# Kernel optimization log

Measured on AMD Instinct MI355X. Metric: run time of the kernel, lower is better.

The kernel has to match this reference:

```python
import jax, jax.numpy as jnp
import numpy as np

B, N, HS = 2, 2048, 1024
H, D = 16, 64
GRID = 16           # crop_size // patch_size
SEG = 20            # d_dim = h_dim = w_dim = 2*(64//3//2)


def setup_inputs() -> dict:
    key = jax.random.key(0)
    ks = jax.random.split(key, 5)
    s = 0.02
    return {
        "hidden_states": jax.random.normal(ks[0], (B, N, HS), jnp.float32),
        "Wq": jax.random.normal(ks[1], (HS, HS), jnp.float32) * s,
        "bq": jnp.zeros((HS,), jnp.float32),
        "Wk": jax.random.normal(ks[2], (HS, HS), jnp.float32) * s,
        "bk": jnp.zeros((HS,), jnp.float32),
        "Wv": jax.random.normal(ks[3], (HS, HS), jnp.float32) * s,
        "bv": jnp.zeros((HS,), jnp.float32),
        "Wp": jax.random.normal(ks[4], (HS, HS), jnp.float32) * s,
        "bp": jnp.zeros((HS,), jnp.float32),
    }


def _rope(x, pos):
    # x: [B, H, N, d], pos: [N] int. Faithful to rotate_queries_or_keys:
    # sin/cos are TILED (concat of two copies), rotation is pairwise interleaved.
    d = x.shape[-1]
    omega = 1.0 / (10000.0 ** (jnp.arange(d // 2, dtype=x.dtype) / (d / 2.0)))
    freq = pos.astype(x.dtype)[:, None] * omega          # [N, d/2]
    sin = jnp.tile(jnp.sin(freq), (1, 2))                # [N, d]
    cos = jnp.tile(jnp.cos(freq), (1, 2))
    xp = x.reshape(x.shape[:-1] + (d // 2, 2))
    rot = jnp.stack([-xp[..., 1], xp[..., 0]], axis=-1).reshape(x.shape)
    return x * cos + rot * sin


def _apply_rope3d(qk, fpos, hpos, wpos):
    parts, s = [], 0
    for pos in (fpos, hpos, wpos):
        parts.append(_rope(qk[..., s:s + SEG], pos))
        s += SEG
    parts.append(qk[..., s:])  # pass-through remainder (4 dims)
    return jnp.concatenate(parts, axis=-1)


def reference(hidden_states, Wq, bq, Wk, bk, Wv, bv, Wp, bp):
    b, n, _ = hidden_states.shape

    def heads(x):  # [B,N,HS] -> [B,H,N,D]
        return x.reshape(b, n, H, D).transpose(0, 2, 1, 3)

    q = heads(hidden_states @ Wq.T + bq)
    k = heads(hidden_states @ Wk.T + bk)
    v = heads(hidden_states @ Wv.T + bv)

    ids = jnp.arange(n)
    tpf = GRID * GRID
    fpos = ids // tpf
    rem = ids - fpos * tpf
    hpos = rem // GRID
    wpos = rem - hpos * GRID

    q = _apply_rope3d(q, fpos, hpos, wpos)
    k = _apply_rope3d(k, fpos, hpos, wpos)

    scores = jnp.einsum('bhqd,bhkd->bhqk', q, k) * (D ** -0.5)
    probs = jax.nn.softmax(scores.astype(jnp.float32), axis=-1).astype(q.dtype)
    ctx = jnp.einsum('bhqk,bhkd->bqhd', probs, v).reshape(b, n, HS)
    return ctx @ Wp.T + bp
```

## Files before the change

kernel.cpp:

```cpp
#include <hip/hip_runtime.h>
#include <hip/hip_bf16.h>
#include <math.h>

#define BB    2
#define NN    2048
#define HSZ   1024
#define NH    16
#define HD    64
#define SEGW  20

#define LOG2E  1.4426950408889634f
#define QSCALE (0.125f * LOG2E)
#define DTHR   8.0f

typedef unsigned short u16;
typedef unsigned int   u32;
using bf16x8 = __attribute__((ext_vector_type(8))) short;
using f32x4  = __attribute__((ext_vector_type(4))) float;

__device__ __forceinline__ u16 f2b(float f) {
    union { float f; u32 u; } x; x.f = f;
    u32 r = x.u + 0x7FFF + ((x.u >> 16) & 1);
    return (u16)(r >> 16);
}
__device__ __forceinline__ u16 f2bc(float f) {
    __hip_bfloat16 h = __float2bfloat16(f);
    return *reinterpret_cast<u16*>(&h);
}

__device__ __forceinline__ void gload16(void* lds, const void* g) {
    __builtin_amdgcn_global_load_lds(
        (const __attribute__((address_space(1))) void*)g,
        (__attribute__((address_space(3))) void*)lds, 16, 0, 0);
}

__global__ __launch_bounds__(256)
void cast_k(const float* __restrict__ hs, const float* __restrict__ Wq,
            const float* __restrict__ Wk, const float* __restrict__ Wv,
            const float* __restrict__ Wp, u16* __restrict__ hsb,
            u16* __restrict__ wqb, u16* __restrict__ wkb,
            u16* __restrict__ wvb, u16* __restrict__ wpb) {
    size_t idx = ((size_t)blockIdx.x * 256 + threadIdx.x) * 4;
    const float* s; u16* d; size_t o;
    const size_t HSN = 4194304, WN = 1048576;
    if      (idx < HSN)          { s = hs; d = hsb; o = idx; }
    else if (idx < HSN + WN)     { s = Wq; d = wqb; o = idx - HSN; }
    else if (idx < HSN + 2*WN)   { s = Wk; d = wkb; o = idx - HSN - WN; }
    else if (idx < HSN + 3*WN)   { s = Wv; d = wvb; o = idx - HSN - 2*WN; }
    else                         { s = Wp; d = wpb; o = idx - HSN - 3*WN; }
    float4 v = *(const float4*)(s + o);
    u32 lo = f2b(v.x) | ((u32)f2b(v.y) << 16);
    u32 hi = f2b(v.z) | ((u32)f2b(v.w) << 16);
    *(uint2*)(d + o) = uint2{lo, hi};
}

__global__ void rope_table_k(float* __restrict__ tab) {
    int n = blockIdx.x, d = threadIdx.x;
    float c = 1.f, s = 0.f;
    if (d < 3 * SEGW) {
        int seg = d / SEGW;
        int jj  = (d % SEGW) % (SEGW / 2);
        int rem = n & 255;
        int pos = (seg == 0) ? (n >> 8) : ((seg == 1) ? (rem >> 4) : (rem & 15));
        float omega = powf(10000.f, -(float)jj / 10.f);
        float fr = (float)pos * omega;
        s = sinf(fr); c = cosf(fr);
    }
    tab[(n * 64 + d) * 2 + 0] = c;
    tab[(n * 64 + d) * 2 + 1] = s;
}

__device__ __forceinline__
void gemm_body(const u16* __restrict__ X, const u16* __restrict__ Wb,
               const float* __restrict__ bias, void* __restrict__ out,
               const float* __restrict__ tab, int mode) {
    __shared__ u16 As[2][128 * 32];
    __shared__ u16 Bs[2][128 * 32];

    const int t  = threadIdx.x;
    const int w  = t >> 6;
    const int l  = t & 63;
    const int o0 = blockIdx.x * 128;
    const int m0 = blockIdx.y * 128;
    const int wr = (w >> 1) * 64;
    const int wc = (w & 1) * 64;

    const int ch  = (w << 6) + l;
    const int rA0 = ch >> 2,         cA0 = (((ch & 3) ^ (rA0 & 3))) * 8;
    const int rA1 = (ch + 256) >> 2, cA1 = (((ch & 3) ^ (rA1 & 3))) * 8;
    const int kbyte = (((l >> 4) ^ (l & 3)) << 4);

    f32x4 acc[4][4] = {};

    gload16(As[0] + ((w << 6)) * 8,       X  + (size_t)(m0 + rA0) * HSZ + cA0);
    gload16(As[0] + (256 + (w << 6)) * 8, X  + (size_t)(m0 + rA1) * HSZ + cA1);
    gload16(Bs[0] + ((w << 6)) * 8,       Wb + (size_t)(o0 + rA0) * HSZ + cA0);
    gload16(Bs[0] + (256 + (w << 6)) * 8, Wb + (size_t)(o0 + rA1) * HSZ + cA1);
    __syncthreads();

    int cur = 0;
    for (int k0 = 0; k0 < HSZ; k0 += 32, cur ^= 1) {
        if (k0 + 32 < HSZ) {
            int kn = k0 + 32;
            gload16(As[cur ^ 1] + ((w << 6)) * 8,       X  + (size_t)(m0 + rA0) * HSZ + kn + cA0);
            gload16(As[cur ^ 1] + (256 + (w << 6)) * 8, X  + (size_t)(m0 + rA1) * HSZ + kn + cA1);
            gload16(Bs[cur ^ 1] + ((w << 6)) * 8,       Wb + (size_t)(o0 + rA0) * HSZ + kn + cA0);
            gload16(Bs[cur ^ 1] + (256 + (w << 6)) * 8, Wb + (size_t)(o0 + rA1) * HSZ + kn + cA1);
        }
        bf16x8 af[4], bfr[4];
#pragma unroll
        for (int i = 0; i < 4; ++i) {
            int row = wr + i * 16 + (l & 15);
            af[i] = *(const bf16x8*)((const char*)As[cur] + row * 64 + kbyte);
        }
#pragma unroll
        for (int j = 0; j < 4; ++j) {
            int row = wc + j * 16 + (l & 15);
            bfr[j] = *(const bf16x8*)((const char*)Bs[cur] + row * 64 + kbyte);
        }
        __builtin_amdgcn_s_setprio(1);
#pragma unroll
        for (int i = 0; i < 4; ++i)
#pragma unroll
            for (int j = 0; j < 4; ++j)
                acc[i][j] = __builtin_amdgcn_mfma_f32_16x16x32_bf16(af[i], bfr[j], acc[i][j], 0, 0, 0);
        __builtin_amdgcn_s_setprio(0);
        __syncthreads();
    }

#pragma unroll
    for (int j = 0; j < 4; ++j) {
        int oc = o0 + wc + j * 16 + (l & 15);
        int h  = oc >> 6;
        int d  = oc & 63;
        float bv = bias[oc];
        if (mode == 2) {
#pragma unroll
            for (int rt = 0; rt < 4; ++rt) {
                int base = m0 + wr + rt * 16 + (l >> 4) * 4;
                int b_ = base >> 11, n0 = base & (NN - 1);
                u16 e[4];
#pragma unroll
                for (int r = 0; r < 4; ++r) e[r] = f2b(acc[rt][j][r] + bv);
                u32 lo = e[0] | ((u32)e[1] << 16);
                u32 hi = e[2] | ((u32)e[3] << 16);
                u16* vp = (u16*)out + (((size_t)b_ * NH + h) * HD + d) * NN + n0;
                *(uint2*)vp = uint2{lo, hi};
            }
        } else if (mode == 3) {
#pragma unroll
            for (int rt = 0; rt < 4; ++rt)
#pragma unroll
                for (int r = 0; r < 4; ++r) {
                    int m = m0 + wr + rt * 16 + (l >> 4) * 4 + r;
                    ((float*)out)[(size_t)m * HSZ + oc] = acc[rt][j][r] + bv;
                }
        } else {
            float scl = (mode == 0) ? QSCALE : 1.f;
#pragma unroll
            for (int rt = 0; rt < 4; ++rt)
#pragma unroll
                for (int r = 0; r < 4; ++r) {
                    int m = m0 + wr + rt * 16 + (l >> 4) * 4 + r;
                    int n = m & (NN - 1), b_ = m >> 11;
                    float v = acc[rt][j][r] + bv;
                    float2 cs = ((const float2*)tab)[n * 64 + d];
                    float part = __shfl_xor(v, 1);
                    float vr = (l & 1) ? fmaf(part, cs.y, v * cs.x)
                                       : fmaf(-part, cs.y, v * cs.x);
                    u16* qp = (u16*)out + (((size_t)b_ * NH + h) * NN + n) * HD + d;
                    *qp = f2b(vr * scl);
                }
        }
    }
}

__global__ __launch_bounds__(256)
void qkv_k(const u16* __restrict__ X,
           const u16* __restrict__ Wq, const u16* __restrict__ Wk, const u16* __restrict__ Wv,
           const float* __restrict__ bq, const float* __restrict__ bk, const float* __restrict__ bv,
           u16* __restrict__ qo, u16* __restrict__ ko, u16* __restrict__ vo,
           const float* __restrict__ tab) {
    int z = blockIdx.z;
    const u16* W   = (z == 0) ? Wq : (z == 1) ? Wk : Wv;
    const float* b = (z == 0) ? bq : (z == 1) ? bk : bv;
    u16* o         = (z == 0) ? qo : (z == 1) ? ko : vo;
    gemm_body(X, W, b, o, tab, z);
}

__global__ __launch_bounds__(256)
void projo_k(const u16* __restrict__ X, const u16* __restrict__ W,
             const float* __restrict__ b, float* __restrict__ out) {
    gemm_body(X, W, b, out, nullptr, 3);
}

__global__ __launch_bounds__(256)
void attn_mfma_k(const u16* __restrict__ Qb, const u16* __restrict__ Kb,
                 const u16* __restrict__ Vtb, u16* __restrict__ ctxb) {
    __shared__ u16 QPs[128 * 64];
    __shared__ u16 Ks[2][64 * 64];
    __shared__ u16 Vs[2][64 * 64];

    const int t = threadIdx.x, w = t >> 6, l = t & 63;
    int f  = blockIdx.y * 16 + blockIdx.x;
    int bh = (f & 7) * 4 + ((f >> 3) & 3);
    int qt = f >> 5;
    const int b_ = bh >> 4, h = bh & 15;

    const u16* Qg  = Qb + ((size_t)bh * NN + qt * 128) * HD;
    const u16* Kg0 = Kb + (size_t)bh * NN * HD;
    const u16* Vg0 = Vtb + (size_t)bh * HD * NN;

    const int ch0 = (w << 6) + l;
    const int r0 = ch0 >> 3,         s0 = (ch0 & 7) ^ (r0 & 7);
    const int r1 = (ch0 + 256) >> 3, s1 = (ch0 & 7) ^ (r1 & 7);

#pragma unroll
    for (int s = 0; s < 4; ++s) {
        int c = s * 256 + ch0;
        int row = c >> 3, sc = (c & 7) ^ (row & 7);
        gload16(QPs + (s * 256 + (w << 6)) * 8, Qg + row * HD + sc * 8);
    }
    gload16(Ks[0] + ((w << 6)) * 8,       Kg0 + (size_t)r0 * HD + s0 * 8);
    gload16(Ks[0] + (256 + (w << 6)) * 8, Kg0 + (size_t)r1 * HD + s1 * 8);
    gload16(Vs[0] + ((w << 6)) * 8,       Vg0 + (size_t)r0 * NN + s0 * 8);
    gload16(Vs[0] + (256 + (w << 6)) * 8, Vg0 + (size_t)r1 * NN + s1 * 8);
    __syncthreads();

    bf16x8 qf[2][2];
#pragma unroll
    for (int qs = 0; qs < 2; ++qs)
#pragma unroll
        for (int kk = 0; kk < 2; ++kk) {
            int row = w * 32 + qs * 16 + (l & 15);
            int cb = (kk * 64 + (l >> 4) * 16) ^ ((row & 7) << 4);
            qf[qs][kk] = *(const bf16x8*)((const char*)QPs + row * 128 + cb);
        }
    __syncthreads();

    bf16x8 ones;
#pragma unroll
    for (int i = 0; i < 8; ++i) ones[i] = (short)0x3F80;

    float m_i[2][4], l_i[2][4] = {};
#pragma unroll
    for (int qs = 0; qs < 2; ++qs)
#pragma unroll
        for (int r = 0; r < 4; ++r) m_i[qs][r] = -INFINITY;
    f32x4 o_acc[2][4] = {};

    int cur = 0;
    for (int kt = 0; kt < NN / 64; ++kt, cur ^= 1) {
        if (kt + 1 < NN / 64) {
            const u16* Kg = Kg0 + (size_t)((kt + 1) * 64) * HD;
            const u16* Vg = Vg0 + (kt + 1) * 64;
            gload16(Ks[cur ^ 1] + ((w << 6)) * 8,       Kg + (size_t)r0 * HD + s0 * 8);
            gload16(Ks[cur ^ 1] + (256 + (w << 6)) * 8, Kg + (size_t)r1 * HD + s1 * 8);
            gload16(Vs[cur ^ 1] + ((w << 6)) * 8,       Vg + (size_t)r0 * NN + s0 * 8);
            gload16(Vs[cur ^ 1] + (256 + (w << 6)) * 8, Vg + (size_t)r1 * NN + s1 * 8);
        }

        f32x4 sacc[2][4] = {};
        __builtin_amdgcn_s_setprio(1);
#pragma unroll
        for (int ct = 0; ct < 4; ++ct) {
            int row = ct * 16 + (l & 15);
#pragma unroll
            for (int kk = 0; kk < 2; ++kk) {
                int cb = (kk * 64 + (l >> 4) * 16) ^ ((row & 7) << 4);
                bf16x8 kf = *(const bf16x8*)((const char*)Ks[cur] + row * 128 + cb);
                sacc[0][ct] = __builtin_amdgcn_mfma_f32_16x16x32_bf16(qf[0][kk], kf, sacc[0][ct], 0, 0, 0);
                sacc[1][ct] = __builtin_amdgcn_mfma_f32_16x16x32_bf16(qf[1][kk], kf, sacc[1][ct], 0, 0, 0);
            }
        }
        __builtin_amdgcn_s_setprio(0);

        float pm[2][4];
        bool grow = false;
#pragma unroll
        for (int qs = 0; qs < 2; ++qs)
#pragma unroll
            for (int r = 0; r < 4; ++r) {
                pm[qs][r] = fmaxf(fmaxf(sacc[qs][0][r], sacc[qs][1][r]),
                                  fmaxf(sacc[qs][2][r], sacc[qs][3][r]));
                grow = grow | (pm[qs][r] > m_i[qs][r] + DTHR);
            }
        if (__any(grow)) {
#pragma unroll
            for (int qs = 0; qs < 2; ++qs)
#pragma unroll
                for (int r = 0; r < 4; ++r) {
                    float mx = pm[qs][r];
                    mx = fmaxf(mx, __shfl_xor(mx, 1));
                    mx = fmaxf(mx, __shfl_xor(mx, 2));
                    mx = fmaxf(mx, __shfl_xor(mx, 4));
                    mx = fmaxf(mx, __shfl_xor(mx, 8));
                    float mn = fmaxf(m_i[qs][r], mx);
                    float alpha = __builtin_amdgcn_exp2f(m_i[qs][r] - mn);
                    m_i[qs][r] = mn;
                    l_i[qs][r] *= alpha;
#pragma unroll
                    for (int dt = 0; dt < 4; ++dt) o_acc[qs][dt][r] *= alpha;
                }
        }

#pragma unroll
        for (int qs = 0; qs < 2; ++qs)
#pragma unroll
            for (int ct = 0; ct < 4; ++ct)
#pragma unroll
                for (int r = 0; r < 4; ++r) {
                    float p = __builtin_amdgcn_exp2f(sacc[qs][ct][r] - m_i[qs][r]);
                    int row = w * 32 + qs * 16 + (l >> 4) * 4 + r;
                    int cb = ((ct * 16 + (l & 15)) * 2) ^ ((row & 7) << 4);
                    *(u16*)((char*)QPs + row * 128 + cb) = f2bc(p);
                }

        f32x4 lacc[2] = {};
        __builtin_amdgcn_s_setprio(1);
#pragma unroll
        for (int kk = 0; kk < 2; ++kk) {
            bf16x8 pf[2];
#pragma unroll
            for (int qs = 0; qs < 2; ++qs) {
                int prow = w * 32 + qs * 16 + (l & 15);
                int pcb = (kk * 64 + (l >> 4) * 16) ^ ((prow & 7) << 4);
                pf[qs] = *(const bf16x8*)((const char*)QPs + prow * 128 + pcb);
            }
            lacc[0] = __builtin_amdgcn_mfma_f32_16x16x32_bf16(pf[0], ones, lacc[0], 0, 0, 0);
            lacc[1] = __builtin_amdgcn_mfma_f32_16x16x32_bf16(pf[1], ones, lacc[1], 0, 0, 0);
#pragma unroll
            for (int dt = 0; dt < 4; ++dt) {
                int vrow = dt * 16 + (l & 15);
                int vcb = (kk * 64 + (l >> 4) * 16) ^ ((vrow & 7) << 4);
                bf16x8 vf = *(const bf16x8*)((const char*)Vs[cur] + vrow * 128 + vcb);
                o_acc[0][dt] = __builtin_amdgcn_mfma_f32_16x16x32_bf16(pf[0], vf, o_acc[0][dt], 0, 0, 0);
                o_acc[1][dt] = __builtin_amdgcn_mfma_f32_16x16x32_bf16(pf[1], vf, o_acc[1][dt], 0, 0, 0);
            }
        }
        __builtin_amdgcn_s_setprio(0);
#pragma unroll
        for (int qs = 0; qs < 2; ++qs)
#pragma unroll
            for (int r = 0; r < 4; ++r) l_i[qs][r] += lacc[qs][r];

        __syncthreads();
    }

#pragma unroll
    for (int qs = 0; qs < 2; ++qs)
#pragma unroll
        for (int r = 0; r < 4; ++r) {
            float inv = 1.f / l_i[qs][r];
            int n = qt * 128 + w * 32 + qs * 16 + (l >> 4) * 4 + r;
#pragma unroll
            for (int dt = 0; dt < 4; ++dt) {
                int d = dt * 16 + (l & 15);
                ctxb[((size_t)b_ * NN + n) * HSZ + h * HD + d] = f2bc(o_acc[qs][dt][r] * inv);
            }
        }
}

extern "C" void kernel_launch(void* const* d_in, const int* in_sizes, int n_in,
                              void* d_out, int out_size, void* d_ws, size_t ws_size,
                              hipStream_t stream) {
    (void)in_sizes; (void)n_in; (void)out_size; (void)ws_size;
    const float* hs = (const float*)d_in[0];
    const float* Wq = (const float*)d_in[1];
    const float* bq = (const float*)d_in[2];
    const float* Wk = (const float*)d_in[3];
    const float* bk = (const float*)d_in[4];
    const float* Wv = (const float*)d_in[5];
    const float* bv = (const float*)d_in[6];
    const float* Wp = (const float*)d_in[7];
    const float* bp = (const float*)d_in[8];

    char* ws = (char*)d_ws;
    u16*   hsb  = (u16*)(ws);
    u16*   Wqb  = (u16*)(ws + 8388608);
    u16*   Wkb  = (u16*)(ws + 10485760);
    u16*   Wvb  = (u16*)(ws + 12582912);
    u16*   Wpb  = (u16*)(ws + 14680064);
    u16*   qb   = (u16*)(ws + 16777216);
    u16*   kb   = (u16*)(ws + 25165824);
    u16*   vtb  = (u16*)(ws + 33554432);
    u16*   ctxb = (u16*)(ws + 41943040);
    float* tab  = (float*)(ws + 50331648);

    cast_k<<<8192, 256, 0, stream>>>(hs, Wq, Wk, Wv, Wp, hsb, Wqb, Wkb, Wvb, Wpb);
    rope_table_k<<<NN, 64, 0, stream>>>(tab);

    qkv_k<<<dim3(HSZ / 128, (BB * NN) / 128, 3), 256, 0, stream>>>(
        hsb, Wqb, Wkb, Wvb, bq, bk, bv, qb, kb, vtb, tab);

    attn_mfma_k<<<dim3(NN / 128, BB * NH), 256, 0, stream>>>(qb, kb, vtb, ctxb);

    projo_k<<<dim3(HSZ / 128, (BB * NN) / 128), 256, 0, stream>>>(ctxb, Wpb, bp, (float*)d_out);
}
```

Before: 150.9 us.

## Split attention over KV halves with a combine kernel, and swizzle GEMM block order

The attention kernel is split along the key sequence into two halves (blockIdx.z). Each half writes unnormalized fp32 partial outputs plus its row max and sum, and a new combine kernel merges them into the bf16 context. Key tiles shrink to 32, LDS use drops, and launch bounds request 4 blocks per CU, all to raise occupancy and parallelism over the previous 512-block grid. The Wp cast moves after attention so its buffer can reuse workspace, and GEMM block indices are remapped for cache locality. The cost is extra fp32 partial traffic and two extra kernel launches.

```diff
diff --git a/kernel.cpp b/kernel.cpp
--- a/kernel.cpp
+++ b/kernel.cpp
@@ -37,21 +37,28 @@
 __global__ __launch_bounds__(256)
 void cast_k(const float* __restrict__ hs, const float* __restrict__ Wq,
             const float* __restrict__ Wk, const float* __restrict__ Wv,
-            const float* __restrict__ Wp, u16* __restrict__ hsb,
-            u16* __restrict__ wqb, u16* __restrict__ wkb,
-            u16* __restrict__ wvb, u16* __restrict__ wpb) {
+            u16* __restrict__ hsb, u16* __restrict__ wqb,
+            u16* __restrict__ wkb, u16* __restrict__ wvb) {
     size_t idx = ((size_t)blockIdx.x * 256 + threadIdx.x) * 4;
     const float* s; u16* d; size_t o;
     const size_t HSN = 4194304, WN = 1048576;
     if      (idx < HSN)          { s = hs; d = hsb; o = idx; }
     else if (idx < HSN + WN)     { s = Wq; d = wqb; o = idx - HSN; }
     else if (idx < HSN + 2*WN)   { s = Wk; d = wkb; o = idx - HSN - WN; }
-    else if (idx < HSN + 3*WN)   { s = Wv; d = wvb; o = idx - HSN - 2*WN; }
-    else                         { s = Wp; d = wpb; o = idx - HSN - 3*WN; }
+    else                         { s = Wv; d = wvb; o = idx - HSN - 2*WN; }
     float4 v = *(const float4*)(s + o);
     u32 lo = f2b(v.x) | ((u32)f2b(v.y) << 16);
     u32 hi = f2b(v.z) | ((u32)f2b(v.w) << 16);
     *(uint2*)(d + o) = uint2{lo, hi};
+}
+
+__global__ __launch_bounds__(256)
+void castwp_k(const float* __restrict__ Wp, u16* __restrict__ wpb) {
+    size_t idx = ((size_t)blockIdx.x * 256 + threadIdx.x) * 4;
+    float4 v = *(const float4*)(Wp + idx);
+    u32 lo = f2b(v.x) | ((u32)f2b(v.y) << 16);
+    u32 hi = f2b(v.z) | ((u32)f2b(v.w) << 16);
+    *(uint2*)(wpb + idx) = uint2{lo, hi};
 }
 
 __global__ void rope_table_k(float* __restrict__ tab) {
@@ -80,8 +87,9 @@
     const int t  = threadIdx.x;
     const int w  = t >> 6;
     const int l  = t & 63;
-    const int o0 = blockIdx.x * 128;
-    const int m0 = blockIdx.y * 128;
+    const int flat = blockIdx.x + (blockIdx.y << 3);
+    const int o0 = (flat >> 5) * 128;
+    const int m0 = (flat & 31) * 128;
     const int wr = (w >> 1) * 64;
     const int wc = (w & 1) * 64;
 
@@ -194,37 +202,39 @@
     gemm_body(X, W, b, out, nullptr, 3);
 }
 
-__global__ __launch_bounds__(256)
+__global__ __launch_bounds__(256, 4)
 void attn_mfma_k(const u16* __restrict__ Qb, const u16* __restrict__ Kb,
-                 const u16* __restrict__ Vtb, u16* __restrict__ ctxb) {
+                 const u16* __restrict__ Vtb, float* __restrict__ po0,
+                 float* __restrict__ po1, float* __restrict__ pm,
+                 float* __restrict__ pl) {
     __shared__ u16 QPs[128 * 64];
-    __shared__ u16 Ks[2][64 * 64];
-    __shared__ u16 Vs[2][64 * 64];
+    __shared__ u16 Ks[2][32 * 64];
+    __shared__ u16 Vs[2][64 * 32];
 
     const int t = threadIdx.x, w = t >> 6, l = t & 63;
     int f  = blockIdx.y * 16 + blockIdx.x;
     int bh = (f & 7) * 4 + ((f >> 3) & 3);
     int qt = f >> 5;
-    const int b_ = bh >> 4, h = bh & 15;
+    const int sp = blockIdx.z;
+    float* po = sp ? po1 : po0;
+    const int kt0 = sp * 32;
 
     const u16* Qg  = Qb + ((size_t)bh * NN + qt * 128) * HD;
     const u16* Kg0 = Kb + (size_t)bh * NN * HD;
     const u16* Vg0 = Vtb + (size_t)bh * HD * NN;
 
-    const int ch0 = (w << 6) + l;
-    const int r0 = ch0 >> 3,         s0 = (ch0 & 7) ^ (r0 & 7);
-    const int r1 = (ch0 + 256) >> 3, s1 = (ch0 & 7) ^ (r1 & 7);
+    const int ch   = (w << 6) + l;
+    const int krow = ch >> 3, ksc = (ch & 7) ^ (krow & 7);
+    const int vrow = ch >> 2, vsc = (ch & 3) ^ (vrow & 3);
 
 #pragma unroll
     for (int s = 0; s < 4; ++s) {
-        int c = s * 256 + ch0;
+        int c = s * 256 + ch;
         int row = c >> 3, sc = (c & 7) ^ (row & 7);
         gload16(QPs + (s * 256 + (w << 6)) * 8, Qg + row * HD + sc * 8);
     }
-    gload16(Ks[0] + ((w << 6)) * 8,       Kg0 + (size_t)r0 * HD + s0 * 8);
-    gload16(Ks[0] + (256 + (w << 6)) * 8, Kg0 + (size_t)r1 * HD + s1 * 8);
-    gload16(Vs[0] + ((w << 6)) * 8,       Vg0 + (size_t)r0 * NN + s0 * 8);
-    gload16(Vs[0] + (256 + (w << 6)) * 8, Vg0 + (size_t)r1 * NN + s1 * 8);
+    gload16(Ks[0] + (w << 6) * 8, Kg0 + (size_t)(kt0 * 32 + krow) * HD + ksc * 8);
+    gload16(Vs[0] + (w << 6) * 8, Vg0 + (size_t)vrow * NN + kt0 * 32 + vsc * 8);
     __syncthreads();
 
     bf16x8 qf[2][2];
@@ -236,7 +246,6 @@
             int cb = (kk * 64 + (l >> 4) * 16) ^ ((row & 7) << 4);
             qf[qs][kk] = *(const bf16x8*)((const char*)QPs + row * 128 + cb);
         }
-    __syncthreads();
 
     bf16x8 ones;
 #pragma unroll
@@ -250,20 +259,18 @@
     f32x4 o_acc[2][4] = {};
 
     int cur = 0;
-    for (int kt = 0; kt < NN / 64; ++kt, cur ^= 1) {
-        if (kt + 1 < NN / 64) {
-            const u16* Kg = Kg0 + (size_t)((kt + 1) * 64) * HD;
-            const u16* Vg = Vg0 + (kt + 1) * 64;
-            gload16(Ks[cur ^ 1] + ((w << 6)) * 8,       Kg + (size_t)r0 * HD + s0 * 8);
-            gload16(Ks[cur ^ 1] + (256 + (w << 6)) * 8, Kg + (size_t)r1 * HD + s1 * 8);
-            gload16(Vs[cur ^ 1] + ((w << 6)) * 8,       Vg + (size_t)r0 * NN + s0 * 8);
-            gload16(Vs[cur ^ 1] + (256 + (w << 6)) * 8, Vg + (size_t)r1 * NN + s1 * 8);
-        }
-
-        f32x4 sacc[2][4] = {};
+    for (int kt = kt0; kt < kt0 + 32; ++kt, cur ^= 1) {
+        if (kt + 1 < kt0 + 32) {
+            gload16(Ks[cur ^ 1] + (w << 6) * 8,
+                    Kg0 + (size_t)((kt + 1) * 32 + krow) * HD + ksc * 8);
+            gload16(Vs[cur ^ 1] + (w << 6) * 8,
+                    Vg0 + (size_t)vrow * NN + (kt + 1) * 32 + vsc * 8);
+        }
+
+        f32x4 sacc[2][2] = {};
         __builtin_amdgcn_s_setprio(1);
 #pragma unroll
-        for (int ct = 0; ct < 4; ++ct) {
+        for (int ct = 0; ct < 2; ++ct) {
             int row = ct * 16 + (l & 15);
 #pragma unroll
             for (int kk = 0; kk < 2; ++kk) {
@@ -275,22 +282,21 @@
         }
         __builtin_amdgcn_s_setprio(0);
 
-        float pm[2][4];
+        float pmx[2][4];
         bool grow = false;
 #pragma unroll
         for (int qs = 0; qs < 2; ++qs)
 #pragma unroll
             for (int r = 0; r < 4; ++r) {
-                pm[qs][r] = fmaxf(fmaxf(sacc[qs][0][r], sacc[qs][1][r]),
-                                  fmaxf(sacc[qs][2][r], sacc[qs][3][r]));
-                grow = grow | (pm[qs][r] > m_i[qs][r] + DTHR);
+                pmx[qs][r] = fmaxf(sacc[qs][0][r], sacc[qs][1][r]);
+                grow = grow | (pmx[qs][r] > m_i[qs][r] + DTHR);
             }
         if (__any(grow)) {
 #pragma unroll
             for (int qs = 0; qs < 2; ++qs)
 #pragma unroll
                 for (int r = 0; r < 4; ++r) {
-                    float mx = pm[qs][r];
+                    float mx = pmx[qs][r];
                     mx = fmaxf(mx, __shfl_xor(mx, 1));
                     mx = fmaxf(mx, __shfl_xor(mx, 2));
                     mx = fmaxf(mx, __shfl_xor(mx, 4));
@@ -307,7 +313,7 @@
 #pragma unroll
         for (int qs = 0; qs < 2; ++qs)
 #pragma unroll
-            for (int ct = 0; ct < 4; ++ct)
+            for (int ct = 0; ct < 2; ++ct)
 #pragma unroll
                 for (int r = 0; r < 4; ++r) {
                     float p = __builtin_amdgcn_exp2f(sacc[qs][ct][r] - m_i[qs][r]);
@@ -317,48 +323,82 @@
                 }
 
         f32x4 lacc[2] = {};
+        bf16x8 pf[2];
+#pragma unroll
+        for (int qs = 0; qs < 2; ++qs) {
+            int prow = w * 32 + qs * 16 + (l & 15);
+            int pcb = ((l >> 4) * 16) ^ ((prow & 7) << 4);
+            pf[qs] = *(const bf16x8*)((const char*)QPs + prow * 128 + pcb);
+        }
         __builtin_amdgcn_s_setprio(1);
-#pragma unroll
-        for (int kk = 0; kk < 2; ++kk) {
-            bf16x8 pf[2];
-#pragma unroll
-            for (int qs = 0; qs < 2; ++qs) {
-                int prow = w * 32 + qs * 16 + (l & 15);
-                int pcb = (kk * 64 + (l >> 4) * 16) ^ ((prow & 7) << 4);
-                pf[qs] = *(const bf16x8*)((const char*)QPs + prow * 128 + pcb);
+        lacc[0] = __builtin_amdgcn_mfma_f32_16x16x32_bf16(pf[0], ones, lacc[0], 0, 0, 0);
+        lacc[1] = __builtin_amdgcn_mfma_f32_16x16x32_bf16(pf[1], ones, lacc[1], 0, 0, 0);
+#pragma unroll
+        for (int dt = 0; dt < 4; ++dt) {
+            int vr = dt * 16 + (l & 15);
+            int vcb = ((l >> 4) * 16) ^ ((vr & 3) << 4);
+            bf16x8 vf = *(const bf16x8*)((const char*)Vs[cur] + vr * 64 + vcb);
+            o_acc[0][dt] = __builtin_amdgcn_mfma_f32_16x16x32_bf16(pf[0], vf, o_acc[0][dt], 0, 0, 0);
+            o_acc[1][dt] = __builtin_amdgcn_mfma_f32_16x16x32_bf16(pf[1], vf, o_acc[1][dt], 0, 0, 0);
+        }
+        __builtin_amdgcn_s_setprio(0);
+#pragma unroll
+        for (int qs = 0; qs < 2; ++qs)
+#pragma unroll
+            for (int r = 0; r < 4; ++r) l_i[qs][r] += lacc[qs][r];
+
+        __syncthreads();
+    }
+
+#pragma unroll
+    for (int qs = 0; qs < 2; ++qs)
+#pragma unroll
+        for (int r = 0; r < 4; ++r) {
+            int n = qt * 128 + w * 32 + qs * 16 + (l >> 4) * 4 + r;
+#pragma unroll
+            for (int dt = 0; dt < 4; ++dt)
+                po[((size_t)bh * NN + n) * HD + dt * 16 + (l & 15)] = o_acc[qs][dt][r];
+        }
+    if ((l & 15) == 0) {
+#pragma unroll
+        for (int qs = 0; qs < 2; ++qs)
+#pragma unroll
+            for (int r = 0; r < 4; ++r) {
+                int n = qt * 128 + w * 32 + qs * 16 + (l >> 4) * 4 + r;
+                pm[sp * 65536 + bh * NN + n] = m_i[qs][r];
+                pl[sp * 65536 + bh * NN + n] = l_i[qs][r];
             }
-            lacc[0] = __builtin_amdgcn_mfma_f32_16x16x32_bf16(pf[0], ones, lacc[0], 0, 0, 0);
-            lacc[1] = __builtin_amdgcn_mfma_f32_16x16x32_bf16(pf[1], ones, lacc[1], 0, 0, 0);
-#pragma unroll
-            for (int dt = 0; dt < 4; ++dt) {
-                int vrow = dt * 16 + (l & 15);
-                int vcb = (kk * 64 + (l >> 4) * 16) ^ ((vrow & 7) << 4);
-                bf16x8 vf = *(const bf16x8*)((const char*)Vs[cur] + vrow * 128 + vcb);
-                o_acc[0][dt] = __builtin_amdgcn_mfma_f32_16x16x32_bf16(pf[0], vf, o_acc[0][dt], 0, 0, 0);
-                o_acc[1][dt] = __builtin_amdgcn_mfma_f32_16x16x32_bf16(pf[1], vf, o_acc[1][dt], 0, 0, 0);
-            }
-        }
-        __builtin_amdgcn_s_setprio(0);
-#pragma unroll
-        for (int qs = 0; qs < 2; ++qs)
-#pragma unroll
-            for (int r = 0; r < 4; ++r) l_i[qs][r] += lacc[qs][r];
-
-        __syncthreads();
-    }
-
-#pragma unroll
-    for (int qs = 0; qs < 2; ++qs)
-#pragma unroll
-        for (int r = 0; r < 4; ++r) {
-            float inv = 1.f / l_i[qs][r];
-            int n = qt * 128 + w * 32 + qs * 16 + (l >> 4) * 4 + r;
-#pragma unroll
-            for (int dt = 0; dt < 4; ++dt) {
-                int d = dt * 16 + (l & 15);
-                ctxb[((size_t)b_ * NN + n) * HSZ + h * HD + d] = f2bc(o_acc[qs][dt][r] * inv);
-            }
-        }
+    }
+}
+
+__global__ __launch_bounds__(256)
+void combine_k(const float* __restrict__ po0, const float* __restrict__ po1,
+               const float* __restrict__ pm, const float* __restrict__ pl,
+               u16* __restrict__ ctxb) {
+    int idx = blockIdx.x * 256 + threadIdx.x;
+    int row = idx >> 2;
+    int dp  = (idx & 3) * 16;
+    int bh = row >> 11, n = row & 2047;
+    int b_ = bh >> 4, h = bh & 15;
+    float m0 = pm[row], m1 = pm[65536 + row];
+    float l0 = pl[row], l1 = pl[65536 + row];
+    float m = fmaxf(m0, m1);
+    float w0 = __builtin_amdgcn_exp2f(m0 - m);
+    float w1 = __builtin_amdgcn_exp2f(m1 - m);
+    float inv = 1.f / (w0 * l0 + w1 * l1);
+    const float* a = po0 + (size_t)row * 64 + dp;
+    const float* b = po1 + (size_t)row * 64 + dp;
+    u16* o = ctxb + ((size_t)b_ * NN + n) * HSZ + h * 64 + dp;
+#pragma unroll
+    for (int j = 0; j < 4; ++j) {
+        float4 x = ((const float4*)a)[j];
+        float4 y = ((const float4*)b)[j];
+        u16 e0 = f2b((x.x * w0 + y.x * w1) * inv);
+        u16 e1 = f2b((x.y * w0 + y.y * w1) * inv);
+        u16 e2 = f2b((x.z * w0 + y.z * w1) * inv);
+        u16 e3 = f2b((x.w * w0 + y.w * w1) * inv);
+        *(uint2*)(o + j * 4) = uint2{e0 | ((u32)e1 << 16), e2 | ((u32)e3 << 16)};
+    }
 }
 
 extern "C" void kernel_launch(void* const* d_in, const int* in_sizes, int n_in,
@@ -380,20 +420,28 @@
     u16*   Wqb  = (u16*)(ws + 8388608);
     u16*   Wkb  = (u16*)(ws + 10485760);
     u16*   Wvb  = (u16*)(ws + 12582912);
-    u16*   Wpb  = (u16*)(ws + 14680064);
     u16*   qb   = (u16*)(ws + 16777216);
     u16*   kb   = (u16*)(ws + 25165824);
     u16*   vtb  = (u16*)(ws + 33554432);
     u16*   ctxb = (u16*)(ws + 41943040);
     float* tab  = (float*)(ws + 50331648);
-
-    cast_k<<<8192, 256, 0, stream>>>(hs, Wq, Wk, Wv, Wp, hsb, Wqb, Wkb, Wvb, Wpb);
+    float* pm   = (float*)(ws + 50331648);
+    float* pl   = (float*)(ws + 50331648 + 524288);
+    float* po0  = (float*)(ws + 51380224);
+    float* po1  = (float*)(ws);
+    u16*   Wpb  = (u16*)(ws);
+
+    cast_k<<<7168, 256, 0, stream>>>(hs, Wq, Wk, Wv, hsb, Wqb, Wkb, Wvb);
     rope_table_k<<<NN, 64, 0, stream>>>(tab);
 
     qkv_k<<<dim3(HSZ / 128, (BB * NN) / 128, 3), 256, 0, stream>>>(
         hsb, Wqb, Wkb, Wvb, bq, bk, bv, qb, kb, vtb, tab);
 
-    attn_mfma_k<<<dim3(NN / 128, BB * NH), 256, 0, stream>>>(qb, kb, vtb, ctxb);
+    attn_mfma_k<<<dim3(NN / 128, BB * NH, 2), 256, 0, stream>>>(
+        qb, kb, vtb, po0, po1, pm, pl);
+
+    combine_k<<<1024, 256, 0, stream>>>(po0, po1, pm, pl, ctxb);
+    castwp_k<<<1024, 256, 0, stream>>>(Wp, Wpb);
 
     projo_k<<<dim3(HSZ / 128, (BB * NN) / 128), 256, 0, stream>>>(ctxb, Wpb, bp, (float*)d_out);
 }
```

New measurement: 162.1 us. 1.07x slower.

## Rewrite attention with 32x32x16 MFMA, transposed scores and register-resident P

Applied to the files above, without the earlier changes.

The attention kernel now computes transposed scores S^T = K·Q^T using 32x32x16 bf16 MFMA, so each lane owns one query row. The softmax row max and sum then reduce in registers with a single cross-half shuffle. The probabilities are packed into bf16 pairs and rearranged with v_permlane32_swap to feed the PV MFMA directly. This removes the LDS round-trip for P, the ones-vector MFMA used for row sums, and the 16-lane shuffle reductions. The GEMM tile mapping is also remapped so that consecutive blocks share weight columns, which should improve L2 reuse.

```diff
diff --git a/kernel.cpp b/kernel.cpp
--- a/kernel.cpp
+++ b/kernel.cpp
@@ -17,6 +17,7 @@
 typedef unsigned int   u32;
 using bf16x8 = __attribute__((ext_vector_type(8))) short;
 using f32x4  = __attribute__((ext_vector_type(4))) float;
+using f32x16 = __attribute__((ext_vector_type(16))) float;
 
 __device__ __forceinline__ u16 f2b(float f) {
     union { float f; u32 u; } x; x.f = f;
@@ -32,6 +33,10 @@
     __builtin_amdgcn_global_load_lds(
         (const __attribute__((address_space(1))) void*)g,
         (__attribute__((address_space(3))) void*)lds, 16, 0, 0);
+}
+
+__device__ __forceinline__ void pswap(u32& a, u32& b) {
+    asm volatile("v_permlane32_swap_b32 %0, %1" : "+v"(a), "+v"(b));
 }
 
 __global__ __launch_bounds__(256)
@@ -80,8 +85,9 @@
     const int t  = threadIdx.x;
     const int w  = t >> 6;
     const int l  = t & 63;
-    const int o0 = blockIdx.x * 128;
-    const int m0 = blockIdx.y * 128;
+    const int flat = blockIdx.x + (blockIdx.y << 3);
+    const int o0 = (flat >> 5) * 128;
+    const int m0 = (flat & 31) * 128;
     const int wr = (w >> 1) * 64;
     const int wc = (w & 1) * 64;
 
@@ -197,168 +203,147 @@
 __global__ __launch_bounds__(256)
 void attn_mfma_k(const u16* __restrict__ Qb, const u16* __restrict__ Kb,
                  const u16* __restrict__ Vtb, u16* __restrict__ ctxb) {
-    __shared__ u16 QPs[128 * 64];
-    __shared__ u16 Ks[2][64 * 64];
-    __shared__ u16 Vs[2][64 * 64];
+    __shared__ u16 KVs[2][2][64 * 64];
 
     const int t = threadIdx.x, w = t >> 6, l = t & 63;
+    const int h = l >> 5;
     int f  = blockIdx.y * 16 + blockIdx.x;
     int bh = (f & 7) * 4 + ((f >> 3) & 3);
     int qt = f >> 5;
-    const int b_ = bh >> 4, h = bh & 15;
-
-    const u16* Qg  = Qb + ((size_t)bh * NN + qt * 128) * HD;
-    const u16* Kg0 = Kb + (size_t)bh * NN * HD;
-    const u16* Vg0 = Vtb + (size_t)bh * HD * NN;
-
-    const int ch0 = (w << 6) + l;
-    const int r0 = ch0 >> 3,         s0 = (ch0 & 7) ^ (r0 & 7);
-    const int r1 = (ch0 + 256) >> 3, s1 = (ch0 & 7) ^ (r1 & 7);
+    const int b_ = bh >> 4, hd = bh & 15;
+
+    const u16* Qg = Qb + ((size_t)bh * NN + qt * 128) * HD;
+    const u16* Kg = Kb + (size_t)bh * NN * HD;
+    const u16* Vg = Vtb + (size_t)bh * HD * NN;
+
+    const int xr   = (l & 7) << 4;
+    const int h16  = h * 16;
+    const int rowo = (l & 31) * 128;
+    int kb4[4];
+#pragma unroll
+    for (int ks = 0; ks < 4; ++ks) kb4[ks] = ((ks * 32) | h16) ^ xr;
+
+    const int ch  = w * 64 + l;
+    const int r0  = ch >> 3,          sl0 = (ch & 7) ^ (r0 & 7);
+    const int r1  = (ch + 256) >> 3,  sl1 = (ch & 7) ^ (r1 & 7);
 
 #pragma unroll
     for (int s = 0; s < 4; ++s) {
-        int c = s * 256 + ch0;
-        int row = c >> 3, sc = (c & 7) ^ (row & 7);
-        gload16(QPs + (s * 256 + (w << 6)) * 8, Qg + row * HD + sc * 8);
-    }
-    gload16(Ks[0] + ((w << 6)) * 8,       Kg0 + (size_t)r0 * HD + s0 * 8);
-    gload16(Ks[0] + (256 + (w << 6)) * 8, Kg0 + (size_t)r1 * HD + s1 * 8);
-    gload16(Vs[0] + ((w << 6)) * 8,       Vg0 + (size_t)r0 * NN + s0 * 8);
-    gload16(Vs[0] + (256 + (w << 6)) * 8, Vg0 + (size_t)r1 * NN + s1 * 8);
+        int c = s * 256 + ch;
+        int row = c >> 3, sl = (c & 7) ^ (row & 7);
+        gload16(&KVs[0][0][0] + (s * 256 + w * 64) * 8, Qg + row * HD + sl * 8);
+    }
     __syncthreads();
-
-    bf16x8 qf[2][2];
-#pragma unroll
-    for (int qs = 0; qs < 2; ++qs)
-#pragma unroll
-        for (int kk = 0; kk < 2; ++kk) {
-            int row = w * 32 + qs * 16 + (l & 15);
-            int cb = (kk * 64 + (l >> 4) * 16) ^ ((row & 7) << 4);
-            qf[qs][kk] = *(const bf16x8*)((const char*)QPs + row * 128 + cb);
-        }
+    bf16x8 qf[4];
+    {
+        const char* Ql = (const char*)&KVs[0][0][0];
+        int qrow = (w * 32 + (l & 31)) * 128;
+#pragma unroll
+        for (int ks = 0; ks < 4; ++ks)
+            qf[ks] = *(const bf16x8*)(Ql + qrow + kb4[ks]);
+    }
     __syncthreads();
 
-    bf16x8 ones;
-#pragma unroll
-    for (int i = 0; i < 8; ++i) ones[i] = (short)0x3F80;
-
-    float m_i[2][4], l_i[2][4] = {};
-#pragma unroll
-    for (int qs = 0; qs < 2; ++qs)
-#pragma unroll
-        for (int r = 0; r < 4; ++r) m_i[qs][r] = -INFINITY;
-    f32x4 o_acc[2][4] = {};
+    gload16(&KVs[0][0][0] + (w * 64) * 8,        Kg + (size_t)r0 * HD + sl0 * 8);
+    gload16(&KVs[0][0][0] + (256 + w * 64) * 8,  Kg + (size_t)r1 * HD + sl1 * 8);
+    gload16(&KVs[0][1][0] + (w * 64) * 8,        Vg + (size_t)r0 * NN + sl0 * 8);
+    gload16(&KVs[0][1][0] + (256 + w * 64) * 8,  Vg + (size_t)r1 * NN + sl1 * 8);
+    __syncthreads();
+
+    float m_i = -INFINITY, l_i = 0.f;
+    f32x16 oa0 = {}, oa1 = {};
 
     int cur = 0;
     for (int kt = 0; kt < NN / 64; ++kt, cur ^= 1) {
         if (kt + 1 < NN / 64) {
-            const u16* Kg = Kg0 + (size_t)((kt + 1) * 64) * HD;
-            const u16* Vg = Vg0 + (kt + 1) * 64;
-            gload16(Ks[cur ^ 1] + ((w << 6)) * 8,       Kg + (size_t)r0 * HD + s0 * 8);
-            gload16(Ks[cur ^ 1] + (256 + (w << 6)) * 8, Kg + (size_t)r1 * HD + s1 * 8);
-            gload16(Vs[cur ^ 1] + ((w << 6)) * 8,       Vg + (size_t)r0 * NN + s0 * 8);
-            gload16(Vs[cur ^ 1] + (256 + (w << 6)) * 8, Vg + (size_t)r1 * NN + s1 * 8);
-        }
-
-        f32x4 sacc[2][4] = {};
+            int nx = (kt + 1) * 64;
+            gload16(&KVs[cur ^ 1][0][0] + (w * 64) * 8,       Kg + (size_t)(nx + r0) * HD + sl0 * 8);
+            gload16(&KVs[cur ^ 1][0][0] + (256 + w * 64) * 8, Kg + (size_t)(nx + r1) * HD + sl1 * 8);
+            gload16(&KVs[cur ^ 1][1][0] + (w * 64) * 8,       Vg + (size_t)r0 * NN + nx + sl0 * 8);
+            gload16(&KVs[cur ^ 1][1][0] + (256 + w * 64) * 8, Vg + (size_t)r1 * NN + nx + sl1 * 8);
+        }
+
+        const char* Kl = (const char*)&KVs[cur][0][0];
+        f32x16 sa0 = {}, sa1 = {};
         __builtin_amdgcn_s_setprio(1);
 #pragma unroll
-        for (int ct = 0; ct < 4; ++ct) {
-            int row = ct * 16 + (l & 15);
-#pragma unroll
-            for (int kk = 0; kk < 2; ++kk) {
-                int cb = (kk * 64 + (l >> 4) * 16) ^ ((row & 7) << 4);
-                bf16x8 kf = *(const bf16x8*)((const char*)Ks[cur] + row * 128 + cb);
-                sacc[0][ct] = __builtin_amdgcn_mfma_f32_16x16x32_bf16(qf[0][kk], kf, sacc[0][ct], 0, 0, 0);
-                sacc[1][ct] = __builtin_amdgcn_mfma_f32_16x16x32_bf16(qf[1][kk], kf, sacc[1][ct], 0, 0, 0);
-            }
+        for (int ks = 0; ks < 4; ++ks) {
+            bf16x8 k0 = *(const bf16x8*)(Kl + rowo + kb4[ks]);
+            bf16x8 k1 = *(const bf16x8*)(Kl + 4096 + rowo + kb4[ks]);
+            sa0 = __builtin_amdgcn_mfma_f32_32x32x16_bf16(k0, qf[ks], sa0, 0, 0, 0);
+            sa1 = __builtin_amdgcn_mfma_f32_32x32x16_bf16(k1, qf[ks], sa1, 0, 0, 0);
         }
         __builtin_amdgcn_s_setprio(0);
 
-        float pm[2][4];
-        bool grow = false;
-#pragma unroll
-        for (int qs = 0; qs < 2; ++qs)
-#pragma unroll
-            for (int r = 0; r < 4; ++r) {
-                pm[qs][r] = fmaxf(fmaxf(sacc[qs][0][r], sacc[qs][1][r]),
-                                  fmaxf(sacc[qs][2][r], sacc[qs][3][r]));
-                grow = grow | (pm[qs][r] > m_i[qs][r] + DTHR);
-            }
-        if (__any(grow)) {
-#pragma unroll
-            for (int qs = 0; qs < 2; ++qs)
-#pragma unroll
-                for (int r = 0; r < 4; ++r) {
-                    float mx = pm[qs][r];
-                    mx = fmaxf(mx, __shfl_xor(mx, 1));
-                    mx = fmaxf(mx, __shfl_xor(mx, 2));
-                    mx = fmaxf(mx, __shfl_xor(mx, 4));
-                    mx = fmaxf(mx, __shfl_xor(mx, 8));
-                    float mn = fmaxf(m_i[qs][r], mx);
-                    float alpha = __builtin_amdgcn_exp2f(m_i[qs][r] - mn);
-                    m_i[qs][r] = mn;
-                    l_i[qs][r] *= alpha;
-#pragma unroll
-                    for (int dt = 0; dt < 4; ++dt) o_acc[qs][dt][r] *= alpha;
-                }
-        }
-
-#pragma unroll
-        for (int qs = 0; qs < 2; ++qs)
-#pragma unroll
-            for (int ct = 0; ct < 4; ++ct)
-#pragma unroll
-                for (int r = 0; r < 4; ++r) {
-                    float p = __builtin_amdgcn_exp2f(sacc[qs][ct][r] - m_i[qs][r]);
-                    int row = w * 32 + qs * 16 + (l >> 4) * 4 + r;
-                    int cb = ((ct * 16 + (l & 15)) * 2) ^ ((row & 7) << 4);
-                    *(u16*)((char*)QPs + row * 128 + cb) = f2bc(p);
-                }
-
-        f32x4 lacc[2] = {};
+        float mx8[8];
+#pragma unroll
+        for (int j = 0; j < 8; ++j)
+            mx8[j] = fmaxf(fmaxf(sa0[j], sa0[j + 8]), fmaxf(sa1[j], sa1[j + 8]));
+        float pm = fmaxf(fmaxf(fmaxf(mx8[0], mx8[1]), fmaxf(mx8[2], mx8[3])),
+                         fmaxf(fmaxf(mx8[4], mx8[5]), fmaxf(mx8[6], mx8[7])));
+        if (__any(pm > m_i + DTHR)) {
+            float mx = fmaxf(pm, __shfl_xor(pm, 32));
+            float mn = fmaxf(m_i, mx);
+            float alpha = __builtin_amdgcn_exp2f(m_i - mn);
+            m_i = mn;
+            l_i *= alpha;
+#pragma unroll
+            for (int r = 0; r < 16; ++r) { oa0[r] *= alpha; oa1[r] *= alpha; }
+        }
+
+        u32 o_[16];
+        float ls0 = 0.f, ls1 = 0.f, ls2 = 0.f, ls3 = 0.f;
+#pragma unroll
+        for (int j = 0; j < 8; ++j) {
+            float pa = __builtin_amdgcn_exp2f(sa0[2 * j]     - m_i);
+            float pb = __builtin_amdgcn_exp2f(sa0[2 * j + 1] - m_i);
+            float pc = __builtin_amdgcn_exp2f(sa1[2 * j]     - m_i);
+            float pd = __builtin_amdgcn_exp2f(sa1[2 * j + 1] - m_i);
+            ls0 += pa; ls1 += pb; ls2 += pc; ls3 += pd;
+            o_[j]     = (u32)f2bc(pa) | ((u32)f2bc(pb) << 16);
+            o_[8 + j] = (u32)f2bc(pc) | ((u32)f2bc(pd) << 16);
+        }
+        l_i += (ls0 + ls1) + (ls2 + ls3);
+
+        pswap(o_[0], o_[2]);   pswap(o_[1], o_[3]);
+        pswap(o_[4], o_[6]);   pswap(o_[5], o_[7]);
+        pswap(o_[8], o_[10]);  pswap(o_[9], o_[11]);
+        pswap(o_[12], o_[14]); pswap(o_[13], o_[15]);
+
+        const char* Vl = (const char*)&KVs[cur][1][0];
         __builtin_amdgcn_s_setprio(1);
 #pragma unroll
-        for (int kk = 0; kk < 2; ++kk) {
-            bf16x8 pf[2];
-#pragma unroll
-            for (int qs = 0; qs < 2; ++qs) {
-                int prow = w * 32 + qs * 16 + (l & 15);
-                int pcb = (kk * 64 + (l >> 4) * 16) ^ ((prow & 7) << 4);
-                pf[qs] = *(const bf16x8*)((const char*)QPs + prow * 128 + pcb);
-            }
-            lacc[0] = __builtin_amdgcn_mfma_f32_16x16x32_bf16(pf[0], ones, lacc[0], 0, 0, 0);
-            lacc[1] = __builtin_amdgcn_mfma_f32_16x16x32_bf16(pf[1], ones, lacc[1], 0, 0, 0);
-#pragma unroll
-            for (int dt = 0; dt < 4; ++dt) {
-                int vrow = dt * 16 + (l & 15);
-                int vcb = (kk * 64 + (l >> 4) * 16) ^ ((vrow & 7) << 4);
-                bf16x8 vf = *(const bf16x8*)((const char*)Vs[cur] + vrow * 128 + vcb);
-                o_acc[0][dt] = __builtin_amdgcn_mfma_f32_16x16x32_bf16(pf[0], vf, o_acc[0][dt], 0, 0, 0);
-                o_acc[1][dt] = __builtin_amdgcn_mfma_f32_16x16x32_bf16(pf[1], vf, o_acc[1][dt], 0, 0, 0);
-            }
+        for (int ks2 = 0; ks2 < 4; ++ks2) {
+            union { u32 u[4]; bf16x8 v; } fr;
+            fr.u[0] = o_[4 * ks2 + 0]; fr.u[1] = o_[4 * ks2 + 1];
+            fr.u[2] = o_[4 * ks2 + 2]; fr.u[3] = o_[4 * ks2 + 3];
+            bf16x8 v0 = *(const bf16x8*)(Vl + rowo + kb4[ks2]);
+            bf16x8 v1 = *(const bf16x8*)(Vl + 4096 + rowo + kb4[ks2]);
+            oa0 = __builtin_amdgcn_mfma_f32_32x32x16_bf16(v0, fr.v, oa0, 0, 0, 0);
+            oa1 = __builtin_amdgcn_mfma_f32_32x32x16_bf16(v1, fr.v, oa1, 0, 0, 0);
         }
         __builtin_amdgcn_s_setprio(0);
-#pragma unroll
-        for (int qs = 0; qs < 2; ++qs)
-#pragma unroll
-            for (int r = 0; r < 4; ++r) l_i[qs][r] += lacc[qs][r];
 
         __syncthreads();
     }
 
-#pragma unroll
-    for (int qs = 0; qs < 2; ++qs)
-#pragma unroll
-        for (int r = 0; r < 4; ++r) {
-            float inv = 1.f / l_i[qs][r];
-            int n = qt * 128 + w * 32 + qs * 16 + (l >> 4) * 4 + r;
-#pragma unroll
-            for (int dt = 0; dt < 4; ++dt) {
-                int d = dt * 16 + (l & 15);
-                ctxb[((size_t)b_ * NN + n) * HSZ + h * HD + d] = f2bc(o_acc[qs][dt][r] * inv);
-            }
-        }
+    float lt = l_i + __shfl_xor(l_i, 32);
+    float inv = 1.f / lt;
+    int n = qt * 128 + w * 32 + (l & 31);
+    u16* op = ctxb + ((size_t)b_ * NN + n) * HSZ + hd * 64;
+#pragma unroll
+    for (int dt = 0; dt < 2; ++dt) {
+        const f32x16& oa = dt ? oa1 : oa0;
+#pragma unroll
+        for (int rg = 0; rg < 4; ++rg) {
+            int d0 = 4 * h + 8 * rg + 32 * dt;
+            u16 e0 = f2bc(oa[4 * rg + 0] * inv);
+            u16 e1 = f2bc(oa[4 * rg + 1] * inv);
+            u16 e2 = f2bc(oa[4 * rg + 2] * inv);
+            u16 e3 = f2bc(oa[4 * rg + 3] * inv);
+            *(uint2*)(op + d0) = uint2{e0 | ((u32)e1 << 16), e2 | ((u32)e3 << 16)};
+        }
+    }
 }
 
 extern "C" void kernel_launch(void* const* d_in, const int* in_sizes, int n_in,
```

Result: faster. 140.4 us (-7.0%).
